# Performance work log

Hardware: AMD Instinct MI355X
Metric: run time of the kernel (lower is better)

The kernel has to match this reference:

```python
import jax, jax.numpy as jnp
import numpy as np

# BEV plane bounds: matches IPM(xbound=[-50,50,0.5], ybound=[-50,50,0.5], z=0, angles=0)
XB = (-50.0, 50.0, 0.5)
YB = (-50.0, 50.0, 0.5)
BEV_W = int((XB[1] - XB[0]) / XB[2])  # 200
BEV_H = int((YB[1] - YB[0]) / YB[2])  # 200


def _plane_xyz():
    """Homogeneous world-plane grid [4, BEV_H*BEV_W] (rotation is identity since angles=0)."""
    x = np.linspace(XB[0], XB[1], BEV_W)
    y = np.linspace(YB[0], YB[1], BEV_H)
    xg, yg = np.meshgrid(x, y)  # (BEV_H, BEV_W)
    xf, yf = xg.flatten(), yg.flatten()
    z = np.zeros_like(xf)  # plane z = 0
    coords = np.stack([yf, xf, z, np.ones_like(xf)], axis=0)
    return jnp.asarray(coords, jnp.float32)


def _rotation_from_euler(roll, pitch, yaw):
    si, sj, sk = np.sin(np.deg2rad([roll, pitch, yaw]))
    ci, cj, ck = np.cos(np.deg2rad([roll, pitch, yaw]))
    cc, cs, sc, ss = ci * ck, ci * sk, si * ck, si * sk
    R = np.identity(4)
    R[0, 0] = cj * ck; R[0, 1] = sj * sc - cs; R[0, 2] = sj * cc + ss
    R[1, 0] = cj * sk; R[1, 1] = sj * ss + cc; R[1, 2] = sj * cs - sc
    R[2, 0] = -sj;     R[2, 1] = cj * si;      R[2, 2] = cj * ci
    return R


def setup_inputs() -> dict:
    key = jax.random.key(0)
    k1, k2, k3 = jax.random.split(key, 3)
    B, N, H, W, C = 2, 6, 128, 352, 32
    images = jax.random.normal(k1, (B, N, H, W, C), jnp.float32)
    # Structured intrinsics (focal 200, principal point at image center) + small noise
    K = np.eye(4); K[0, 0] = 200.0; K[1, 1] = 200.0; K[0, 2] = W / 2.0; K[1, 2] = H / 2.0
    Ks = np.tile(K[None], (B * N, 1, 1))
    yaws = [0.0, 60.0, 120.0, 180.0, 240.0, 300.0]
    RTs = np.zeros((B * N, 4, 4))
    for i in range(B * N):
        R = _rotation_from_euler(0.0, -90.0, yaws[i % N])  # camera looking down at plane
        R[2, 3] = 2.0  # camera height
        RTs[i] = R
    Ks = jnp.asarray(Ks, jnp.float32) + 0.01 * jax.random.normal(k2, (B * N, 4, 4), jnp.float32)
    RTs = jnp.asarray(RTs, jnp.float32) + 0.001 * jax.random.normal(k3, (B * N, 4, 4), jnp.float32)
    return {"images": images, "Ks": Ks, "RTs": RTs}


def _ipm_forward(images, Ks, RTs):
    B, N, H, W, C = images.shape
    BN = B * N
    imgs = images.reshape(BN, H, W, C)
    xyz = _plane_xyz()  # [4, h*w]
    h, w = BEV_H, BEV_W
    eps = 1e-7
    # Perspective projection: P @ xyz -> pixel coords [BN, h, w, 2]
    P = (Ks @ RTs).reshape(-1, 4, 4)
    pc = P @ xyz  # [BN, 4, h*w]
    pix = pc[:, :2, :] / (pc[:, 2:3, :] + eps)  # [BN, 2, h*w]
    pix = pix.reshape(BN, 2, h, w).transpose(0, 2, 3, 1)  # [BN, h, w, 2]
    # Bilinear sampling (clamp-to-border, matching the torch code ordering:
    # floor -> clip corners -> weights from CLIPPED corners)
    pix_x = pix[..., 0:1]
    pix_y = pix[..., 1:2]
    x0 = jnp.floor(pix_x); x1 = x0 + 1.0
    y0 = jnp.floor(pix_y); y1 = y0 + 1.0
    x_max, y_max = float(W - 1), float(H - 1)
    x0 = jnp.clip(x0, 0.0, x_max); x1 = jnp.clip(x1, 0.0, x_max)
    y0 = jnp.clip(y0, 0.0, y_max); y1 = jnp.clip(y1, 0.0, y_max)
    wt_x0 = x1 - pix_x; wt_x1 = pix_x - x0
    wt_y0 = y1 - pix_y; wt_y1 = pix_y - y0
    base_y0 = y0 * W; base_y1 = y1 * W
    imgs_flat = imgs.reshape(BN, H * W, C)
    def gather(flat_idx):  # flat_idx: [BN, h, w, 1] float -> gathered [BN, h, w, C]
        idx = flat_idx.reshape(BN, -1, 1).astype(jnp.int32)
        return jnp.take_along_axis(imgs_flat, idx, axis=1).reshape(BN, h, w, C)
    im00 = gather(x0 + base_y0)
    im01 = gather(x0 + base_y1)
    im10 = gather(x1 + base_y0)
    im11 = gather(x1 + base_y1)
    out = (wt_x0 * wt_y0) * im00 + (wt_x0 * wt_y1) * im01 \
        + (wt_x1 * wt_y0) * im10 + (wt_x1 * wt_y1) * im11
    out = out.reshape(B, N, h, w, C)
    return out.max(axis=1)  # [B, h, w, C]


def reference(images, Ks, RTs):
    return _ipm_forward(images, Ks, RTs)
```

## Files before the change

kernel.cpp:

```cpp
#include <hip/hip_runtime.h>
#include <math.h>

#define NUM_CAM   12
#define CAM_PER_B 6
#define IMG_H     128
#define IMG_W     352
#define CH        32
#define BEV       200
#define PIX_PER_B (BEV * BEV)
#define PIX_PER_BLOCK 32
#define BLOCKS_PER_B (PIX_PER_B / PIX_PER_BLOCK)

typedef float vfloat4 __attribute__((ext_vector_type(4)));

__global__ __launch_bounds__(256, 6) void ipm_kernel(
    const float* __restrict__ imgs,
    const float* __restrict__ Ks,
    const float* __restrict__ RTs,
    float* __restrict__ out)
{
    __shared__ float sw00[CAM_PER_B][PIX_PER_BLOCK];
    __shared__ float sw01[CAM_PER_B][PIX_PER_BLOCK];
    __shared__ float sw10[CAM_PER_B][PIX_PER_BLOCK];
    __shared__ float sw11[CAM_PER_B][PIX_PER_BLOCK];
    __shared__ int   soff[CAM_PER_B][PIX_PER_BLOCK];

    const int tid = threadIdx.x;
    const int b = blockIdx.x / BLOCKS_PER_B;

    if (tid < CAM_PER_B * PIX_PER_BLOCK) {
        const int cam = tid >> 5;
        const int pix = tid & 31;
        const int pix_id = blockIdx.x * PIX_PER_BLOCK + pix;
        const int rem = pix_id - b * PIX_PER_B;
        const int gy = rem / BEV;
        const int gx = rem - gy * BEV;

        const double step = 100.0 / 199.0;
        const float xf = (float)(-50.0 + (double)gx * step);
        const float yf = (float)(-50.0 + (double)gy * step);

        const int cg = b * CAM_PER_B + cam;
        const float* K  = Ks  + cg * 16;
        const float* RT = RTs + cg * 16;

        float P[9];
        #pragma unroll
        for (int r = 0; r < 3; ++r) {
            #pragma unroll
            for (int cc = 0; cc < 3; ++cc) {
                const int col = (cc == 2) ? 3 : cc;
                float acc = 0.0f;
                #pragma unroll
                for (int kk = 0; kk < 4; ++kk)
                    acc += K[r * 4 + kk] * RT[kk * 4 + col];
                P[r * 3 + cc] = acc;
            }
        }

        const float den = (P[6] * yf + P[7] * xf + P[8]) + 1e-7f;
        const float px  = (P[0] * yf + P[1] * xf + P[2]) / den;
        const float py  = (P[3] * yf + P[4] * xf + P[5]) / den;

        const float x0f = floorf(px);
        const float y0f = floorf(py);

        const bool valid = (x0f >= 0.0f) & (x0f <= (float)(IMG_W - 2)) &
                           (y0f >= 0.0f) & (y0f <= (float)(IMG_H - 2));

        sw10[cam][pix] = px - x0f;
        sw00[cam][pix] = (x0f + 1.0f) - px;
        sw11[cam][pix] = py - y0f;
        sw01[cam][pix] = (y0f + 1.0f) - py;

        int off = -1;
        if (valid) {
            const int xi = (int)x0f;
            const int yi = (int)y0f;
            off = ((cg * IMG_H + yi) * IMG_W + xi) * CH;
        }
        soff[cam][pix] = off;
    }
    __syncthreads();

    const int pix = tid >> 3;
    const int c4  = (tid & 7) * 4;
    const int pix_id = blockIdx.x * PIX_PER_BLOCK + pix;

    float4 best = make_float4(-INFINITY, -INFINITY, -INFINITY, -INFINITY);

    #pragma unroll
    for (int n = 0; n < CAM_PER_B; ++n) {
        const int off = soff[n][pix];
        float4 val = make_float4(0.0f, 0.0f, 0.0f, 0.0f);
        if (off >= 0) {
            const float wx0 = sw00[n][pix];
            const float wy0 = sw01[n][pix];
            const float wx1 = sw10[n][pix];
            const float wy1 = sw11[n][pix];

            const float* base = imgs + off + c4;
            const float4 a00 = *(const float4*)(base);
            const float4 a10 = *(const float4*)(base + CH);
            const float4 a01 = *(const float4*)(base + IMG_W * CH);
            const float4 a11 = *(const float4*)(base + IMG_W * CH + CH);

            const float c00 = wx0 * wy0;
            const float c01 = wx0 * wy1;
            const float c10 = wx1 * wy0;
            const float c11 = wx1 * wy1;

            val.x = ((c00 * a00.x + c01 * a01.x) + c10 * a10.x) + c11 * a11.x;
            val.y = ((c00 * a00.y + c01 * a01.y) + c10 * a10.y) + c11 * a11.y;
            val.z = ((c00 * a00.z + c01 * a01.z) + c10 * a10.z) + c11 * a11.z;
            val.w = ((c00 * a00.w + c01 * a01.w) + c10 * a10.w) + c11 * a11.w;
        }
        best.x = fmaxf(best.x, val.x);
        best.y = fmaxf(best.y, val.y);
        best.z = fmaxf(best.z, val.z);
        best.w = fmaxf(best.w, val.w);
    }

    vfloat4 bv;
    bv.x = best.x; bv.y = best.y; bv.z = best.z; bv.w = best.w;
    __builtin_nontemporal_store(bv, (vfloat4*)(out + (size_t)pix_id * CH + c4));
}

extern "C" void kernel_launch(void* const* d_in, const int* in_sizes, int n_in,
                              void* d_out, int out_size, void* d_ws, size_t ws_size,
                              hipStream_t stream) {
    const float* images = (const float*)d_in[0];
    const float* Ks     = (const float*)d_in[1];
    const float* RTs    = (const float*)d_in[2];
    float* out          = (float*)d_out;

    const int total_blocks = 2 * BLOCKS_PER_B;
    ipm_kernel<<<total_blocks, 256, 0, stream>>>(images, Ks, RTs, out);
}
```

Baseline: 99.19 us.

## Compact valid camera list per pixel, tile BEV 8x4, remap blocks per XCD

Each pixel now builds a compacted list of only the cameras that project inside the image, using an LDS atomic counter, with the bilinear weights precomputed. The gather loop then runs only up to the wave's maximum valid count and processes two cameras per iteration. BEV pixels are tiled 8x4 instead of linear rows, and block IDs are remapped so that consecutive tiles land on the same XCD, which should improve L2 locality. The risks are extra shared-memory atomics and barriers, and divergence when pixels in a wave have different valid counts. Initialising the max to 0 when fewer than six cameras are valid reproduces the zero contribution from invalid cameras.

Result: no change. 99.48 us (+0.3%).

```diff
diff --git a/kernel.cpp b/kernel.cpp
--- a/kernel.cpp
+++ b/kernel.cpp
@@ -7,11 +7,21 @@
 #define IMG_W     352
 #define CH        32
 #define BEV       200
-#define PIX_PER_B (BEV * BEV)
+#define TILE_X    8
+#define TILE_Y    4
+#define TILES_X   (BEV / TILE_X)
+#define TILES_Y   (BEV / TILE_Y)
+#define TILES_PER_B (TILES_X * TILES_Y)
+#define NWG       (2 * TILES_PER_B)
 #define PIX_PER_BLOCK 32
-#define BLOCKS_PER_B (PIX_PER_B / PIX_PER_BLOCK)
 
 typedef float vfloat4 __attribute__((ext_vector_type(4)));
+
+struct __align__(16) Entry {
+    float c00, c01, c10, c11;
+    int   off;
+    int   pad0, pad1, pad2;
+};
 
 __global__ __launch_bounds__(256, 6) void ipm_kernel(
     const float* __restrict__ imgs,
@@ -19,22 +29,34 @@
     const float* __restrict__ RTs,
     float* __restrict__ out)
 {
-    __shared__ float sw00[CAM_PER_B][PIX_PER_BLOCK];
-    __shared__ float sw01[CAM_PER_B][PIX_PER_BLOCK];
-    __shared__ float sw10[CAM_PER_B][PIX_PER_BLOCK];
-    __shared__ float sw11[CAM_PER_B][PIX_PER_BLOCK];
-    __shared__ int   soff[CAM_PER_B][PIX_PER_BLOCK];
+    __shared__ Entry slist[CAM_PER_B][PIX_PER_BLOCK];
+    __shared__ int   scnt[PIX_PER_BLOCK];
 
     const int tid = threadIdx.x;
-    const int b = blockIdx.x / BLOCKS_PER_B;
+
+    {
+    }
+    const int wg  = blockIdx.x;
+    const int q   = NWG >> 3;
+    const int r   = NWG & 7;
+    const int xcd = wg & 7;
+    const int ix  = wg >> 3;
+    const int L   = (xcd < r) ? (xcd * (q + 1) + ix)
+                              : (r * (q + 1) + (xcd - r) * q + ix);
+
+    const int b  = L / TILES_PER_B;
+    const int t  = L - b * TILES_PER_B;
+    const int by = t / TILES_X;
+    const int bx = t - by * TILES_X;
+
+    if (tid < PIX_PER_BLOCK) scnt[tid] = 0;
+    __syncthreads();
 
     if (tid < CAM_PER_B * PIX_PER_BLOCK) {
         const int cam = tid >> 5;
         const int pix = tid & 31;
-        const int pix_id = blockIdx.x * PIX_PER_BLOCK + pix;
-        const int rem = pix_id - b * PIX_PER_B;
-        const int gy = rem / BEV;
-        const int gx = rem - gy * BEV;
+        const int gx = bx * TILE_X + (pix & 7);
+        const int gy = by * TILE_Y + (pix >> 3);
 
         const double step = 100.0 / 199.0;
         const float xf = (float)(-50.0 + (double)gx * step);
@@ -46,15 +68,15 @@
 
         float P[9];
         #pragma unroll
-        for (int r = 0; r < 3; ++r) {
+        for (int rr = 0; rr < 3; ++rr) {
             #pragma unroll
             for (int cc = 0; cc < 3; ++cc) {
                 const int col = (cc == 2) ? 3 : cc;
                 float acc = 0.0f;
                 #pragma unroll
                 for (int kk = 0; kk < 4; ++kk)
-                    acc += K[r * 4 + kk] * RT[kk * 4 + col];
-                P[r * 3 + cc] = acc;
+                    acc += K[rr * 4 + kk] * RT[kk * 4 + col];
+                P[rr * 3 + cc] = acc;
             }
         }
 
@@ -68,62 +90,84 @@
         const bool valid = (x0f >= 0.0f) & (x0f <= (float)(IMG_W - 2)) &
                            (y0f >= 0.0f) & (y0f <= (float)(IMG_H - 2));
 
-        sw10[cam][pix] = px - x0f;
-        sw00[cam][pix] = (x0f + 1.0f) - px;
-        sw11[cam][pix] = py - y0f;
-        sw01[cam][pix] = (y0f + 1.0f) - py;
-
-        int off = -1;
         if (valid) {
+            const float wx1 = px - x0f;
+            const float wx0 = (x0f + 1.0f) - px;
+            const float wy1 = py - y0f;
+            const float wy0 = (y0f + 1.0f) - py;
             const int xi = (int)x0f;
             const int yi = (int)y0f;
-            off = ((cg * IMG_H + yi) * IMG_W + xi) * CH;
+            const int off = ((cg * IMG_H + yi) * IMG_W + xi) * CH;
+
+            const int slot = atomicAdd(&scnt[pix], 1);
+            float4 cprod;
+            cprod.x = wx0 * wy0;
+            cprod.y = wx0 * wy1;
+            cprod.z = wx1 * wy0;
+            cprod.w = wx1 * wy1;
+            *(float4*)&slist[slot][pix] = cprod;
+            slist[slot][pix].off = off;
         }
-        soff[cam][pix] = off;
     }
     __syncthreads();
 
     const int pix = tid >> 3;
     const int c4  = (tid & 7) * 4;
-    const int pix_id = blockIdx.x * PIX_PER_BLOCK + pix;
+    const int gx = bx * TILE_X + (pix & 7);
+    const int gy = by * TILE_Y + (pix >> 3);
 
-    float4 best = make_float4(-INFINITY, -INFINITY, -INFINITY, -INFINITY);
+    const int k = scnt[pix];
+    int kw = k;
+    kw = max(kw, __shfl_xor(kw, 8));
+    kw = max(kw, __shfl_xor(kw, 16));
+    kw = max(kw, __shfl_xor(kw, 32));
 
-    #pragma unroll
-    for (int n = 0; n < CAM_PER_B; ++n) {
-        const int off = soff[n][pix];
-        float4 val = make_float4(0.0f, 0.0f, 0.0f, 0.0f);
-        if (off >= 0) {
-            const float wx0 = sw00[n][pix];
-            const float wy0 = sw01[n][pix];
-            const float wx1 = sw10[n][pix];
-            const float wy1 = sw11[n][pix];
+    const float binit = (k == 6) ? -INFINITY : 0.0f;
+    float4 best = make_float4(binit, binit, binit, binit);
 
-            const float* base = imgs + off + c4;
-            const float4 a00 = *(const float4*)(base);
-            const float4 a10 = *(const float4*)(base + CH);
-            const float4 a01 = *(const float4*)(base + IMG_W * CH);
-            const float4 a11 = *(const float4*)(base + IMG_W * CH + CH);
+    for (int j = 0; j < kw; j += 2) {
+        float4 cA = *(const float4*)&slist[j][pix];
+        int offA  = slist[j][pix].off;
+        float4 cB = *(const float4*)&slist[j + 1][pix];
+        int offB  = slist[j + 1][pix].off;
 
-            const float c00 = wx0 * wy0;
-            const float c01 = wx0 * wy1;
-            const float c10 = wx1 * wy0;
-            const float c11 = wx1 * wy1;
+        const bool aAct = (j < k);
+        const bool bAct = (j + 1 < k);
+        if (!aAct) { cA = make_float4(0.f, 0.f, 0.f, 0.f); offA = 0; }
+        if (!bAct) { cB = make_float4(0.f, 0.f, 0.f, 0.f); offB = 0; }
 
-            val.x = ((c00 * a00.x + c01 * a01.x) + c10 * a10.x) + c11 * a11.x;
-            val.y = ((c00 * a00.y + c01 * a01.y) + c10 * a10.y) + c11 * a11.y;
-            val.z = ((c00 * a00.z + c01 * a01.z) + c10 * a10.z) + c11 * a11.z;
-            val.w = ((c00 * a00.w + c01 * a01.w) + c10 * a10.w) + c11 * a11.w;
-        }
-        best.x = fmaxf(best.x, val.x);
-        best.y = fmaxf(best.y, val.y);
-        best.z = fmaxf(best.z, val.z);
-        best.w = fmaxf(best.w, val.w);
+        const float* pA = imgs + offA + c4;
+        const float* pB = imgs + offB + c4;
+        const float4 a00 = *(const float4*)(pA);
+        const float4 a10 = *(const float4*)(pA + CH);
+        const float4 a01 = *(const float4*)(pA + IMG_W * CH);
+        const float4 a11 = *(const float4*)(pA + IMG_W * CH + CH);
+        const float4 e00 = *(const float4*)(pB);
+        const float4 e10 = *(const float4*)(pB + CH);
+        const float4 e01 = *(const float4*)(pB + IMG_W * CH);
+        const float4 e11 = *(const float4*)(pB + IMG_W * CH + CH);
+
+        float4 vA, vB;
+        vA.x = ((cA.x * a00.x + cA.y * a01.x) + cA.z * a10.x) + cA.w * a11.x;
+        vA.y = ((cA.x * a00.y + cA.y * a01.y) + cA.z * a10.y) + cA.w * a11.y;
+        vA.z = ((cA.x * a00.z + cA.y * a01.z) + cA.z * a10.z) + cA.w * a11.z;
+        vA.w = ((cA.x * a00.w + cA.y * a01.w) + cA.z * a10.w) + cA.w * a11.w;
+
+        vB.x = ((cB.x * e00.x + cB.y * e01.x) + cB.z * e10.x) + cB.w * e11.x;
+        vB.y = ((cB.x * e00.y + cB.y * e01.y) + cB.z * e10.y) + cB.w * e11.y;
+        vB.z = ((cB.x * e00.z + cB.y * e01.z) + cB.z * e10.z) + cB.w * e11.z;
+        vB.w = ((cB.x * e00.w + cB.y * e01.w) + cB.z * e10.w) + cB.w * e11.w;
+
+        best.x = fmaxf(fmaxf(best.x, vA.x), vB.x);
+        best.y = fmaxf(fmaxf(best.y, vA.y), vB.y);
+        best.z = fmaxf(fmaxf(best.z, vA.z), vB.z);
+        best.w = fmaxf(fmaxf(best.w, vA.w), vB.w);
     }
 
+    const size_t o = ((size_t)(b * BEV + gy) * BEV + gx) * CH + c4;
     vfloat4 bv;
     bv.x = best.x; bv.y = best.y; bv.z = best.z; bv.w = best.w;
-    __builtin_nontemporal_store(bv, (vfloat4*)(out + (size_t)pix_id * CH + c4));
+    __builtin_nontemporal_store(bv, (vfloat4*)(out + o));
 }
 
 extern "C" void kernel_launch(void* const* d_in, const int* in_sizes, int n_in,
@@ -134,6 +178,5 @@
     const float* RTs    = (const float*)d_in[2];
     float* out          = (float*)d_out;
 
-    const int total_blocks = 2 * BLOCKS_PER_B;
-    ipm_kernel<<<total_blocks, 256, 0, stream>>>(images, Ks, RTs, out);
+    ipm_kernel<<<NWG, 256, 0, stream>>>(images, Ks, RTs, out);
 }
```
